# Kernel optimization log

Hardware: AMD Instinct MI355X
Metric: run time of the kernel (lower is better)

The kernel has to match this reference:

```python
import jax, jax.numpy as jnp
import numpy as np

EMBED_DIM = 1024
NUM_HEADS = 16
HEAD_DIM = EMBED_DIM // NUM_HEADS
B, S = 8, 1024


def setup_inputs() -> dict:
    key = jax.random.key(0)
    ks = jax.random.split(key, 8)
    scale = 1.0 / np.sqrt(EMBED_DIM)
    return {
        "q": jax.random.normal(ks[0], (B, S, EMBED_DIM), jnp.float32),
        "v": jax.random.normal(ks[1], (B, S, EMBED_DIM), jnp.float32),
        "Wq": jax.random.normal(ks[2], (EMBED_DIM, EMBED_DIM), jnp.float32) * scale,
        "bq": jnp.zeros((EMBED_DIM,), jnp.float32),
        "Wk": jax.random.normal(ks[3], (EMBED_DIM, EMBED_DIM), jnp.float32) * scale,
        "bk": jnp.zeros((EMBED_DIM,), jnp.float32),
        "Wv": jax.random.normal(ks[4], (EMBED_DIM, EMBED_DIM), jnp.float32) * scale,
        "bv": jnp.zeros((EMBED_DIM,), jnp.float32),
    }


def reference(q, v, Wq, bq, Wk, bk, Wv, bv):
    # call(q, v, k=None): k defaults to v, then compute_multihead_attention(q, v, k)
    # maps (q_arg=q, k_arg=v, v_arg=v) in self-attention.
    qp = q @ Wq + bq                     # [B, S, E]
    kp = v @ Wk + bk                     # [B, S, E]
    vp = v @ Wv + bv                     # [B, S, E]
    # split along feature dim into heads (same math as tf.split+concat on batch)
    qh = qp.reshape(B, S, NUM_HEADS, HEAD_DIM)
    kh = kp.reshape(B, S, NUM_HEADS, HEAD_DIM)
    vh = vp.reshape(B, S, NUM_HEADS, HEAD_DIM)
    # NOTE: original scales by 1/sqrt(embed_dim), not 1/sqrt(head_dim)
    scores = jnp.einsum("bqhd,bkhd->bhqk", qh, kh) / np.sqrt(EMBED_DIM)
    att = jax.nn.softmax(scores, axis=-1)
    out = jnp.einsum("bhqk,bkhd->bqhd", att, vh)  # [B, S, H, Dh]
    return out.reshape(B, S, EMBED_DIM)
```

## Files before the change

### kernel.cpp

```cpp
#include <hip/hip_runtime.h>
#include <cstdint>
#include <cstddef>

#define E 1024
#define S 1024
#define NB 8
#define NH 16
#define DH 64

typedef __bf16 bf16_t;
typedef __bf16 bf16x8 __attribute__((ext_vector_type(8)));
typedef __bf16 bf16x4 __attribute__((ext_vector_type(4)));
typedef __bf16 bf16x2 __attribute__((ext_vector_type(2)));
typedef short s16x4 __attribute__((ext_vector_type(4)));
typedef float f32x4 __attribute__((ext_vector_type(4)));

static __device__ __forceinline__ void gload_lds16(const void* g, void* l) {
  __builtin_amdgcn_global_load_lds((const __attribute__((address_space(1))) void*)g,
                                   (__attribute__((address_space(3))) void*)l, 16, 0, 0);
}

static __device__ __forceinline__ float fast_exp2(float x) {
#if __has_builtin(__builtin_amdgcn_exp2f)
  return __builtin_amdgcn_exp2f(x);
#else
  float r;
  asm("v_exp_f32 %0, %1" : "=v"(r) : "v"(x));
  return r;
#endif
}

__global__ __launch_bounds__(256) void convert_kernel(
    const float* __restrict__ q, const float* __restrict__ v,
    bf16_t* __restrict__ qb, bf16_t* __restrict__ vb) {
  const float* src = blockIdx.y ? v : q;
  bf16_t* dst = blockIdx.y ? vb : qb;
  const size_t i = ((size_t)blockIdx.x * 256 + threadIdx.x) * 8;
  float4 a = *(const float4*)(src + i);
  float4 b = *(const float4*)(src + i + 4);
  bf16x8 o = {(bf16_t)a.x, (bf16_t)a.y, (bf16_t)a.z, (bf16_t)a.w,
              (bf16_t)b.x, (bf16_t)b.y, (bf16_t)b.z, (bf16_t)b.w};
  *(bf16x8*)(dst + i) = o;
}

__global__ void wtrans_kernel(const float* __restrict__ Wq, const float* __restrict__ Wk,
                              const float* __restrict__ Wv, bf16_t* __restrict__ Wqt,
                              bf16_t* __restrict__ Wkt, bf16_t* __restrict__ Wvt) {
  const float* W = (blockIdx.z == 0) ? Wq : (blockIdx.z == 1) ? Wk : Wv;
  bf16_t* Wt = (blockIdx.z == 0) ? Wqt : (blockIdx.z == 1) ? Wkt : Wvt;
  __shared__ float tile[32][33];
  const int n0 = blockIdx.x * 32, k0 = blockIdx.y * 32;
  const int tx = threadIdx.x, ty = threadIdx.y;
#pragma unroll
  for (int i = ty; i < 32; i += 8)
    tile[i][tx] = W[(size_t)(k0 + i) * E + n0 + tx];
  __syncthreads();
#pragma unroll
  for (int i = ty; i < 32; i += 8)
    Wt[(size_t)(n0 + i) * E + k0 + tx] = (bf16_t)tile[tx][i];
}

__global__ __launch_bounds__(256, 2) void gemm3_kernel(
    const bf16_t* __restrict__ qbf, const bf16_t* __restrict__ vbf,
    const bf16_t* __restrict__ Wqt, const bf16_t* __restrict__ Wkt,
    const bf16_t* __restrict__ Wvt, const float* __restrict__ bq,
    const float* __restrict__ bk, const float* __restrict__ bv,
    bf16_t* __restrict__ qp, bf16_t* __restrict__ kp, bf16_t* __restrict__ vp,
    float qscale) {
  extern __shared__ __align__(16) char smem[];

  const int t = threadIdx.x;
  const int wv = t >> 6, l = t & 63;
  const int lc = l & 15, lg = l >> 4;
  const int wc = wv;

  const int nt = blockIdx.y;
  const int sel = nt >> 2;
  const bf16_t* A = sel ? vbf : qbf;
  const bf16_t* Bt = (sel == 0) ? Wqt : (sel == 1) ? Wkt : Wvt;
  const float* bias = (sel == 0) ? bq : (sel == 1) ? bk : bv;
  bf16_t* C = (sel == 0) ? qp : (sel == 1) ? kp : vp;
  const float scale = (sel == 0) ? qscale : 1.0f;

  const int m0 = blockIdx.x * 128;
  const int n0 = (nt & 3) * 256;

  const int rr = t >> 2;
  const int sgE = ((((t & 3) + ((t >> 3) & 3)) & 3)) << 3;
  const bf16_t* aS0 = A + (size_t)(m0 + rr) * E + sgE;
  const bf16_t* aS1 = A + (size_t)(m0 + 64 + rr) * E + sgE;
  const bf16_t* bS0 = Bt + (size_t)(n0 + rr) * E + sgE;
  const bf16_t* bS1 = Bt + (size_t)(n0 + 64 + rr) * E + sgE;
  const bf16_t* bS2 = Bt + (size_t)(n0 + 128 + rr) * E + sgE;
  const bf16_t* bS3 = Bt + (size_t)(n0 + 192 + rr) * E + sgE;

#define STAGE(tile, buf)                          \
  {                                               \
    const int k0_ = (tile) * 32;                  \
    char* d_ = smem + (buf) * 24576 + wv * 1024;  \
    gload_lds16(aS0 + k0_, d_);                   \
    gload_lds16(aS1 + k0_, d_ + 4096);            \
    gload_lds16(bS0 + k0_, d_ + 8192);            \
    gload_lds16(bS1 + k0_, d_ + 12288);           \
    gload_lds16(bS2 + k0_, d_ + 16384);           \
    gload_lds16(bS3 + k0_, d_ + 20480);           \
  }

  const int cRd = ((lg - (lc >> 1)) & 3) << 4;
  const int aRowB = lc * 64 + cRd;
  const int bRowB = 8192 + (wc * 64 + lc) * 64 + cRd;

  f32x4 acc[8][4] = {};

  STAGE(0, 0);
  STAGE(1, 1);
  asm volatile("s_waitcnt vmcnt(6)" ::: "memory");
  asm volatile("s_barrier" ::: "memory");

  int bufC = 0, bufS = 2;
  for (int tk = 0; tk < 32; ++tk) {
    const char* base = smem + bufC * 24576;
    if (tk + 2 < 32) STAGE(tk + 2, bufS);

    bf16x8 fa[8], fb[4];
#pragma unroll
    for (int ni = 0; ni < 4; ++ni)
      fb[ni] = *(const bf16x8*)(base + bRowB + ni * 1024);
#pragma unroll
    for (int mi = 0; mi < 8; ++mi)
      fa[mi] = *(const bf16x8*)(base + aRowB + mi * 1024);

    __builtin_amdgcn_s_setprio(1);
#pragma unroll
    for (int mi = 0; mi < 8; ++mi)
#pragma unroll
      for (int ni = 0; ni < 4; ++ni)
        acc[mi][ni] = __builtin_amdgcn_mfma_f32_16x16x32_bf16(fa[mi], fb[ni], acc[mi][ni], 0, 0, 0);
    __builtin_amdgcn_s_setprio(0);

    if (tk + 2 < 32) {
      asm volatile("s_waitcnt vmcnt(6)" ::: "memory");
    } else if (tk == 30) {
      asm volatile("s_waitcnt vmcnt(0)" ::: "memory");
    }
    if (tk < 31) asm volatile("s_barrier" ::: "memory");
    bufC = (bufC == 2) ? 0 : bufC + 1;
    bufS = (bufS == 2) ? 0 : bufS + 1;
  }
#undef STAGE

#pragma unroll
  for (int ni = 0; ni < 4; ++ni) {
    const int n = n0 + wc * 64 + ni * 16 + lc;
    const float bv_ = bias[n];
#pragma unroll
    for (int mi = 0; mi < 8; ++mi) {
#pragma unroll
      for (int r = 0; r < 4; ++r) {
        const int m = m0 + mi * 16 + lg * 4 + r;
        C[(size_t)m * E + n] = (bf16_t)((acc[mi][ni][r] + bv_) * scale);
      }
    }
  }
}

#if __has_builtin(__builtin_amdgcn_mfma_f32_16x16x16bf16_1k)
static __device__ __forceinline__ f32x4 mfma16(s16x4 a, s16x4 b, f32x4 c) {
  return __builtin_amdgcn_mfma_f32_16x16x16bf16_1k(a, b, c, 0, 0, 0);
}
#else
static __device__ __forceinline__ f32x4 mfma16(s16x4 a, s16x4 b, f32x4 c) {
  asm volatile("v_mfma_f32_16x16x16_bf16 %0, %1, %2, %0" : "+v"(c) : "v"(a), "v"(b));
  return c;
}
#endif

__global__ __launch_bounds__(256, 2) void attn_kernel(
    const bf16_t* __restrict__ qp, const bf16_t* __restrict__ kp,
    const bf16_t* __restrict__ vp, float* __restrict__ out) {
  __shared__ __align__(16) unsigned char KsB[2][64 * 128];
  __shared__ bf16_t Vs[2][64][72];
  const int t = threadIdx.x;
  const int w = t >> 6, l = t & 63;
  const int lc = l & 15, lg = l >> 4;

  const int swz = (blockIdx.x & 7) * 64 + (blockIdx.x >> 3);
  const int qblk = swz & 3, bh = swz >> 2;
  const int h = bh & 15, b = bh >> 4;
  const int qbase = qblk * 256 + w * 64;
  const size_t bh_off = (size_t)b * S * E + (size_t)h * DH;

  bf16x8 qf[4][2];
#pragma unroll
  for (int qi = 0; qi < 4; ++qi)
#pragma unroll
    for (int kc = 0; kc < 2; ++kc)
      qf[qi][kc] = *(const bf16x8*)(qp + bh_off + (size_t)(qbase + 16 * qi + lc) * E + kc * 32 + lg * 8);

  f32x4 po[4][4] = {};
  float l_[4] = {0.f, 0.f, 0.f, 0.f};

  const int krow = t >> 2, kc4 = t & 3;
  const int vkv2 = (t & 31) * 2, vd0 = (t >> 5) * 8;
  const bf16_t* kbase = kp + bh_off;
  const bf16_t* vbase = vp + bh_off;
  const int ksw = (krow & 7) << 4;

  bf16x8 ka0, ka1, va0, va1;
  {
    const bf16_t* ks = kbase + (size_t)krow * E + kc4 * 16;
    ka0 = *(const bf16x8*)ks;
    ka1 = *(const bf16x8*)(ks + 8);
    const bf16_t* vs = vbase + (size_t)vkv2 * E + vd0;
    va0 = *(const bf16x8*)vs;
    va1 = *(const bf16x8*)(vs + E);
    *(bf16x8*)&KsB[0][krow * 128 + ((kc4 * 32) ^ ksw)] = ka0;
    *(bf16x8*)&KsB[0][krow * 128 + ((kc4 * 32 + 16) ^ ksw)] = ka1;
#pragma unroll
    for (int j = 0; j < 8; ++j) {
      bf16x2 pr;
      pr[0] = va0[j];
      pr[1] = va1[j];
      *(bf16x2*)&Vs[0][vd0 + j][vkv2] = pr;
    }
  }
  int cur = 0;

  for (int kv0 = 0; kv0 < S; kv0 += 64) {
    __syncthreads();

    const bool more = (kv0 + 64 < S);
    if (more) {
      const bf16_t* ks = kbase + (size_t)(kv0 + 64 + krow) * E + kc4 * 16;
      ka0 = *(const bf16x8*)ks;
      ka1 = *(const bf16x8*)(ks + 8);
      const bf16_t* vs = vbase + (size_t)(kv0 + 64 + vkv2) * E + vd0;
      va0 = *(const bf16x8*)vs;
      va1 = *(const bf16x8*)(vs + E);
    }

    s16x4 pa[4][4];
    __builtin_amdgcn_s_setprio(1);
#pragma unroll
    for (int kvb = 0; kvb < 4; ++kvb) {
      const int row = kvb * 16 + lc;
      const int sw = (lc & 7) << 4;
      bf16x8 ak0 = *(const bf16x8*)&KsB[cur][row * 128 + ((lg * 16) ^ sw)];
      bf16x8 ak1 = *(const bf16x8*)&KsB[cur][row * 128 + ((64 + lg * 16) ^ sw)];
      f32x4 sc[4] = {};
#pragma unroll
      for (int qi = 0; qi < 4; ++qi) {
        sc[qi] = __builtin_amdgcn_mfma_f32_16x16x32_bf16(ak0, qf[qi][0], sc[qi], 0, 0, 0);
        sc[qi] = __builtin_amdgcn_mfma_f32_16x16x32_bf16(ak1, qf[qi][1], sc[qi], 0, 0, 0);
      }
#pragma unroll
      for (int qi = 0; qi < 4; ++qi) {
        const float e0 = fast_exp2(sc[qi][0]);
        const float e1 = fast_exp2(sc[qi][1]);
        const float e2 = fast_exp2(sc[qi][2]);
        const float e3 = fast_exp2(sc[qi][3]);
        l_[qi] += (e0 + e1) + (e2 + e3);
        bf16x4 pb = {(bf16_t)e0, (bf16_t)e1, (bf16_t)e2, (bf16_t)e3};
        pa[qi][kvb] = *(s16x4*)&pb;
      }
    }

#pragma unroll
    for (int ki = 0; ki < 4; ++ki) {
      s16x4 av[4];
#pragma unroll
      for (int ni = 0; ni < 4; ++ni)
        av[ni] = *(const s16x4*)&Vs[cur][16 * ni + lc][16 * ki + lg * 4];
#pragma unroll
      for (int qi = 0; qi < 4; ++qi)
#pragma unroll
        for (int ni = 0; ni < 4; ++ni)
          po[qi][ni] = mfma16(av[ni], pa[qi][ki], po[qi][ni]);
    }
    __builtin_amdgcn_s_setprio(0);

    if (more) {
      const int nb_ = cur ^ 1;
      *(bf16x8*)&KsB[nb_][krow * 128 + ((kc4 * 32) ^ ksw)] = ka0;
      *(bf16x8*)&KsB[nb_][krow * 128 + ((kc4 * 32 + 16) ^ ksw)] = ka1;
#pragma unroll
      for (int j = 0; j < 8; ++j) {
        bf16x2 pr;
        pr[0] = va0[j];
        pr[1] = va1[j];
        *(bf16x2*)&Vs[nb_][vd0 + j][vkv2] = pr;
      }
      cur = nb_;
    }
  }

#pragma unroll
  for (int qi = 0; qi < 4; ++qi) {
    float lt = l_[qi];
    lt += __shfl_xor(lt, 16, 64);
    lt += __shfl_xor(lt, 32, 64);
    const float inv = 1.0f / lt;
    const int qrow = qbase + 16 * qi + lc;
    float* op = out + (size_t)b * S * E + (size_t)qrow * E + h * DH;
#pragma unroll
    for (int ni = 0; ni < 4; ++ni) {
      f32x4 r = po[qi][ni] * inv;
      *(f32x4*)(op + 16 * ni + lg * 4) = r;
    }
  }
}

extern "C" void kernel_launch(void* const* d_in, const int* in_sizes, int n_in,
                              void* d_out, int out_size, void* d_ws, size_t ws_size,
                              hipStream_t stream) {
  const float* q  = (const float*)d_in[0];
  const float* v  = (const float*)d_in[1];
  const float* Wq = (const float*)d_in[2];
  const float* bq = (const float*)d_in[3];
  const float* Wk = (const float*)d_in[4];
  const float* bk = (const float*)d_in[5];
  const float* Wv = (const float*)d_in[6];
  const float* bv = (const float*)d_in[7];
  float* out = (float*)d_out;

  char* ws = (char*)d_ws;
  bf16_t* Wqt = (bf16_t*)(ws);
  bf16_t* Wkt = (bf16_t*)(ws + (size_t)2 * 1024 * 1024);
  bf16_t* Wvt = (bf16_t*)(ws + (size_t)4 * 1024 * 1024);
  bf16_t* qp  = (bf16_t*)(ws + (size_t)6 * 1024 * 1024);
  bf16_t* kp  = (bf16_t*)(ws + (size_t)22 * 1024 * 1024);
  bf16_t* vp  = (bf16_t*)(ws + (size_t)38 * 1024 * 1024);

  bf16_t* qbf = (bf16_t*)d_out;
  bf16_t* vbf = qbf + (size_t)NB * S * E;

  (void)hipFuncSetAttribute((const void*)gemm3_kernel,
                            hipFuncAttributeMaxDynamicSharedMemorySize, 73728);

  convert_kernel<<<dim3(4096, 2), 256, 0, stream>>>(q, v, qbf, vbf);
  wtrans_kernel<<<dim3(32, 32, 3), dim3(32, 8), 0, stream>>>(Wq, Wk, Wv, Wqt, Wkt, Wvt);

  const float qscale = 0.03125f * 1.44269504088896f;
  gemm3_kernel<<<dim3(64, 12), 256, 73728, stream>>>(qbf, vbf, Wqt, Wkt, Wvt,
                                                     bq, bk, bv, qp, kp, vp, qscale);
  attn_kernel<<<dim3(512), 256, 0, stream>>>(qp, kp, vp, out);
}
```

Measured before the change: 135.3 us.

## Fuse fp32-to-bf16 input conversion into projection GEMM and use 16x16x32 MFMA for PV

```diff
diff --git a/kernel.cpp b/kernel.cpp
--- a/kernel.cpp
+++ b/kernel.cpp
@@ -30,19 +30,6 @@
 #endif
 }
 
-__global__ __launch_bounds__(256) void convert_kernel(
-    const float* __restrict__ q, const float* __restrict__ v,
-    bf16_t* __restrict__ qb, bf16_t* __restrict__ vb) {
-  const float* src = blockIdx.y ? v : q;
-  bf16_t* dst = blockIdx.y ? vb : qb;
-  const size_t i = ((size_t)blockIdx.x * 256 + threadIdx.x) * 8;
-  float4 a = *(const float4*)(src + i);
-  float4 b = *(const float4*)(src + i + 4);
-  bf16x8 o = {(bf16_t)a.x, (bf16_t)a.y, (bf16_t)a.z, (bf16_t)a.w,
-              (bf16_t)b.x, (bf16_t)b.y, (bf16_t)b.z, (bf16_t)b.w};
-  *(bf16x8*)(dst + i) = o;
-}
-
 __global__ void wtrans_kernel(const float* __restrict__ Wq, const float* __restrict__ Wk,
                               const float* __restrict__ Wv, bf16_t* __restrict__ Wqt,
                               bf16_t* __restrict__ Wkt, bf16_t* __restrict__ Wvt) {
@@ -61,7 +48,7 @@
 }
 
 __global__ __launch_bounds__(256, 2) void gemm3_kernel(
-    const bf16_t* __restrict__ qbf, const bf16_t* __restrict__ vbf,
+    const float* __restrict__ qf32, const float* __restrict__ vf32,
     const bf16_t* __restrict__ Wqt, const bf16_t* __restrict__ Wkt,
     const bf16_t* __restrict__ Wvt, const float* __restrict__ bq,
     const float* __restrict__ bk, const float* __restrict__ bv,
@@ -76,7 +63,7 @@
 
   const int nt = blockIdx.y;
   const int sel = nt >> 2;
-  const bf16_t* A = sel ? vbf : qbf;
+  const float* A = sel ? vf32 : qf32;
   const bf16_t* Bt = (sel == 0) ? Wqt : (sel == 1) ? Wkt : Wvt;
   const float* bias = (sel == 0) ? bq : (sel == 1) ? bk : bv;
   bf16_t* C = (sel == 0) ? qp : (sel == 1) ? kp : vp;
@@ -86,24 +73,54 @@
   const int n0 = (nt & 3) * 256;
 
   const int rr = t >> 2;
-  const int sgE = ((((t & 3) + ((t >> 3) & 3)) & 3)) << 3;
-  const bf16_t* aS0 = A + (size_t)(m0 + rr) * E + sgE;
-  const bf16_t* aS1 = A + (size_t)(m0 + 64 + rr) * E + sgE;
-  const bf16_t* bS0 = Bt + (size_t)(n0 + rr) * E + sgE;
-  const bf16_t* bS1 = Bt + (size_t)(n0 + 64 + rr) * E + sgE;
-  const bf16_t* bS2 = Bt + (size_t)(n0 + 128 + rr) * E + sgE;
-  const bf16_t* bS3 = Bt + (size_t)(n0 + 192 + rr) * E + sgE;
-
-#define STAGE(tile, buf)                          \
+  const int sg = ((t & 3) + ((t >> 3) & 3)) & 3;
+  const float* aF0 = A + (size_t)(m0 + rr) * E + sg * 8;
+  const float* aF1 = A + (size_t)(m0 + 64 + rr) * E + sg * 8;
+  const bf16_t* bS0 = Bt + (size_t)(n0 + rr) * E + sg * 8;
+  const bf16_t* bS1 = Bt + (size_t)(n0 + 64 + rr) * E + sg * 8;
+  const bf16_t* bS2 = Bt + (size_t)(n0 + 128 + rr) * E + sg * 8;
+  const bf16_t* bS3 = Bt + (size_t)(n0 + 192 + rr) * E + sg * 8;
+  char* const aw0base = smem + t * 16;
+  char* const aw1base = smem + 4096 + t * 16;
+
+  f32x4 raE[4], raO[4];
+
+#define AISSUE(ra, tile)                          \
+  {                                               \
+    const float* f0_ = aF0 + (tile) * 32;         \
+    const float* f1_ = aF1 + (tile) * 32;         \
+    ra[0] = *(const f32x4*)f0_;                   \
+    ra[1] = *(const f32x4*)(f0_ + 4);             \
+    ra[2] = *(const f32x4*)f1_;                   \
+    ra[3] = *(const f32x4*)(f1_ + 4);             \
+  }
+
+#define AWRITE(ra, buf)                                                      \
+  {                                                                          \
+    bf16x8 w0_ = {(bf16_t)ra[0][0], (bf16_t)ra[0][1], (bf16_t)ra[0][2],      \
+                  (bf16_t)ra[0][3], (bf16_t)ra[1][0], (bf16_t)ra[1][1],      \
+                  (bf16_t)ra[1][2], (bf16_t)ra[1][3]};                       \
+    bf16x8 w1_ = {(bf16_t)ra[2][0], (bf16_t)ra[2][1], (bf16_t)ra[2][2],      \
+                  (bf16_t)ra[2][3], (bf16_t)ra[3][0], (bf16_t)ra[3][1],      \
+                  (bf16_t)ra[3][2], (bf16_t)ra[3][3]};                       \
+    *(bf16x8*)(aw0base + (buf) * 24576) = w0_;                               \
+    *(bf16x8*)(aw1base + (buf) * 24576) = w1_;                               \
+  }
+
+#define BSTAGE(tile, buf)                         \
   {                                               \
     const int k0_ = (tile) * 32;                  \
-    char* d_ = smem + (buf) * 24576 + wv * 1024;  \
-    gload_lds16(aS0 + k0_, d_);                   \
-    gload_lds16(aS1 + k0_, d_ + 4096);            \
-    gload_lds16(bS0 + k0_, d_ + 8192);            \
-    gload_lds16(bS1 + k0_, d_ + 12288);           \
-    gload_lds16(bS2 + k0_, d_ + 16384);           \
-    gload_lds16(bS3 + k0_, d_ + 20480);           \
+    char* d_ = smem + (buf) * 24576 + 8192 + wv * 1024; \
+    gload_lds16(bS0 + k0_, d_);                   \
+    gload_lds16(bS1 + k0_, d_ + 4096);            \
+    gload_lds16(bS2 + k0_, d_ + 8192);            \
+    gload_lds16(bS3 + k0_, d_ + 12288);           \
+  }
+
+#define BARW()                                              \
+  {                                                         \
+    asm volatile("s_waitcnt lgkmcnt(0)" ::: "memory");      \
+    __builtin_amdgcn_s_barrier();                           \
   }
 
   const int cRd = ((lg - (lc >> 1)) & 3) << 4;
@@ -112,42 +129,68 @@
 
   f32x4 acc[8][4] = {};
 
-  STAGE(0, 0);
-  STAGE(1, 1);
-  asm volatile("s_waitcnt vmcnt(6)" ::: "memory");
-  asm volatile("s_barrier" ::: "memory");
-
-  int bufC = 0, bufS = 2;
-  for (int tk = 0; tk < 32; ++tk) {
-    const char* base = smem + bufC * 24576;
-    if (tk + 2 < 32) STAGE(tk + 2, bufS);
-
-    bf16x8 fa[8], fb[4];
-#pragma unroll
-    for (int ni = 0; ni < 4; ++ni)
-      fb[ni] = *(const bf16x8*)(base + bRowB + ni * 1024);
-#pragma unroll
-    for (int mi = 0; mi < 8; ++mi)
-      fa[mi] = *(const bf16x8*)(base + aRowB + mi * 1024);
-
-    __builtin_amdgcn_s_setprio(1);
-#pragma unroll
-    for (int mi = 0; mi < 8; ++mi)
-#pragma unroll
-      for (int ni = 0; ni < 4; ++ni)
-        acc[mi][ni] = __builtin_amdgcn_mfma_f32_16x16x32_bf16(fa[mi], fb[ni], acc[mi][ni], 0, 0, 0);
-    __builtin_amdgcn_s_setprio(0);
-
+#define COMPUTE(base)                                                        \
+  {                                                                          \
+    bf16x8 fa[8], fb[4];                                                     \
+    _Pragma("unroll") for (int ni = 0; ni < 4; ++ni)                         \
+        fb[ni] = *(const bf16x8*)((base) + bRowB + ni * 1024);               \
+    _Pragma("unroll") for (int mi = 0; mi < 8; ++mi)                         \
+        fa[mi] = *(const bf16x8*)((base) + aRowB + mi * 1024);               \
+    __builtin_amdgcn_s_setprio(1);                                           \
+    _Pragma("unroll") for (int mi = 0; mi < 8; ++mi)                         \
+        _Pragma("unroll") for (int ni = 0; ni < 4; ++ni)                     \
+            acc[mi][ni] = __builtin_amdgcn_mfma_f32_16x16x32_bf16(           \
+                fa[mi], fb[ni], acc[mi][ni], 0, 0, 0);                       \
+    __builtin_amdgcn_s_setprio(0);                                           \
+  }
+
+  AISSUE(raE, 0);
+  BSTAGE(0, 0);
+  AISSUE(raO, 1);
+  BSTAGE(1, 1);
+  asm volatile("s_waitcnt vmcnt(12)" ::: "memory");
+  AWRITE(raE, 0);
+  asm volatile("s_waitcnt vmcnt(8)" ::: "memory");
+  BARW();
+
+  int bc = 0;
+  for (int tk = 0; tk < 32; tk += 2) {
+    const int b1 = (bc + 1 == 3) ? 0 : bc + 1;
+    const int b2 = (b1 + 1 == 3) ? 0 : b1 + 1;
     if (tk + 2 < 32) {
-      asm volatile("s_waitcnt vmcnt(6)" ::: "memory");
-    } else if (tk == 30) {
+      AISSUE(raE, tk + 2);
+      BSTAGE(tk + 2, b2);
+    }
+    COMPUTE(smem + bc * 24576);
+    if (tk + 2 < 32) {
+      asm volatile("s_waitcnt vmcnt(12)" ::: "memory");
+      AWRITE(raO, b1);
+      asm volatile("s_waitcnt vmcnt(8)" ::: "memory");
+      BARW();
+    } else {
+      asm volatile("s_waitcnt vmcnt(4)" ::: "memory");
+      AWRITE(raO, b1);
       asm volatile("s_waitcnt vmcnt(0)" ::: "memory");
-    }
-    if (tk < 31) asm volatile("s_barrier" ::: "memory");
-    bufC = (bufC == 2) ? 0 : bufC + 1;
-    bufS = (bufS == 2) ? 0 : bufS + 1;
-  }
-#undef STAGE
+      BARW();
+    }
+    if (tk + 3 < 32) {
+      AISSUE(raO, tk + 3);
+      BSTAGE(tk + 3, bc);
+    }
+    COMPUTE(smem + b1 * 24576);
+    if (tk + 3 < 32) {
+      asm volatile("s_waitcnt vmcnt(12)" ::: "memory");
+      AWRITE(raE, b2);
+      asm volatile("s_waitcnt vmcnt(8)" ::: "memory");
+      BARW();
+    }
+    bc = b2;
+  }
+#undef COMPUTE
+#undef BARW
+#undef BSTAGE
+#undef AWRITE
+#undef AISSUE
 
 #pragma unroll
   for (int ni = 0; ni < 4; ++ni) {
@@ -163,17 +206,6 @@
     }
   }
 }
-
-#if __has_builtin(__builtin_amdgcn_mfma_f32_16x16x16bf16_1k)
-static __device__ __forceinline__ f32x4 mfma16(s16x4 a, s16x4 b, f32x4 c) {
-  return __builtin_amdgcn_mfma_f32_16x16x16bf16_1k(a, b, c, 0, 0, 0);
-}
-#else
-static __device__ __forceinline__ f32x4 mfma16(s16x4 a, s16x4 b, f32x4 c) {
-  asm volatile("v_mfma_f32_16x16x16_bf16 %0, %1, %2, %0" : "+v"(c) : "v"(a), "v"(b));
-  return c;
-}
-#endif
 
 __global__ __launch_bounds__(256, 2) void attn_kernel(
     const bf16_t* __restrict__ qp, const bf16_t* __restrict__ kp,
@@ -239,7 +271,7 @@
       va1 = *(const bf16x8*)(vs + E);
     }
 
-    s16x4 pa[4][4];
+    bf16x8 pa2[4][2];
     __builtin_amdgcn_s_setprio(1);
 #pragma unroll
     for (int kvb = 0; kvb < 4; ++kvb) {
@@ -260,22 +292,28 @@
         const float e2 = fast_exp2(sc[qi][2]);
         const float e3 = fast_exp2(sc[qi][3]);
         l_[qi] += (e0 + e1) + (e2 + e3);
-        bf16x4 pb = {(bf16_t)e0, (bf16_t)e1, (bf16_t)e2, (bf16_t)e3};
-        pa[qi][kvb] = *(s16x4*)&pb;
-      }
-    }
-
-#pragma unroll
-    for (int ki = 0; ki < 4; ++ki) {
-      s16x4 av[4];
-#pragma unroll
-      for (int ni = 0; ni < 4; ++ni)
-        av[ni] = *(const s16x4*)&Vs[cur][16 * ni + lc][16 * ki + lg * 4];
+        const int hi = (kvb & 1) * 4;
+        pa2[qi][kvb >> 1][hi + 0] = (bf16_t)e0;
+        pa2[qi][kvb >> 1][hi + 1] = (bf16_t)e1;
+        pa2[qi][kvb >> 1][hi + 2] = (bf16_t)e2;
+        pa2[qi][kvb >> 1][hi + 3] = (bf16_t)e3;
+      }
+    }
+
+#pragma unroll
+    for (int ki = 0; ki < 2; ++ki) {
+      bf16x8 av[4];
+#pragma unroll
+      for (int ni = 0; ni < 4; ++ni) {
+        const bf16x4 vlo = *(const bf16x4*)&Vs[cur][16 * ni + lc][32 * ki + 4 * lg];
+        const bf16x4 vhi = *(const bf16x4*)&Vs[cur][16 * ni + lc][32 * ki + 16 + 4 * lg];
+        av[ni] = __builtin_shufflevector(vlo, vhi, 0, 1, 2, 3, 4, 5, 6, 7);
+      }
 #pragma unroll
       for (int qi = 0; qi < 4; ++qi)
 #pragma unroll
         for (int ni = 0; ni < 4; ++ni)
-          po[qi][ni] = mfma16(av[ni], pa[qi][ki], po[qi][ni]);
+          po[qi][ni] = __builtin_amdgcn_mfma_f32_16x16x32_bf16(av[ni], pa2[qi][ki], po[qi][ni], 0, 0, 0);
     }
     __builtin_amdgcn_s_setprio(0);
 
@@ -331,17 +369,13 @@
   bf16_t* kp  = (bf16_t*)(ws + (size_t)22 * 1024 * 1024);
   bf16_t* vp  = (bf16_t*)(ws + (size_t)38 * 1024 * 1024);
 
-  bf16_t* qbf = (bf16_t*)d_out;
-  bf16_t* vbf = qbf + (size_t)NB * S * E;
-
   (void)hipFuncSetAttribute((const void*)gemm3_kernel,
                             hipFuncAttributeMaxDynamicSharedMemorySize, 73728);
 
-  convert_kernel<<<dim3(4096, 2), 256, 0, stream>>>(q, v, qbf, vbf);
   wtrans_kernel<<<dim3(32, 32, 3), dim3(32, 8), 0, stream>>>(Wq, Wk, Wv, Wqt, Wkt, Wvt);
 
   const float qscale = 0.03125f * 1.44269504088896f;
-  gemm3_kernel<<<dim3(64, 12), 256, 73728, stream>>>(qbf, vbf, Wqt, Wkt, Wvt,
+  gemm3_kernel<<<dim3(64, 12), 256, 73728, stream>>>(q, v, Wqt, Wkt, Wvt,
                                                      bq, bk, bv, qp, kp, vp, qscale);
   attn_kernel<<<dim3(512), 256, 0, stream>>>(qp, kp, vp, out);
 }
```

Measured after the change: 118.7 us. 12.3% less time.

## Merge prep kernels and use 16x16x32 MFMA for PV product

Applied to the files above, without the earlier changes.

```diff
diff --git a/kernel.cpp b/kernel.cpp
--- a/kernel.cpp
+++ b/kernel.cpp
@@ -30,27 +30,31 @@
 #endif
 }
 
-__global__ __launch_bounds__(256) void convert_kernel(
+__global__ __launch_bounds__(256) void prep_kernel(
     const float* __restrict__ q, const float* __restrict__ v,
-    bf16_t* __restrict__ qb, bf16_t* __restrict__ vb) {
-  const float* src = blockIdx.y ? v : q;
-  bf16_t* dst = blockIdx.y ? vb : qb;
-  const size_t i = ((size_t)blockIdx.x * 256 + threadIdx.x) * 8;
-  float4 a = *(const float4*)(src + i);
-  float4 b = *(const float4*)(src + i + 4);
-  bf16x8 o = {(bf16_t)a.x, (bf16_t)a.y, (bf16_t)a.z, (bf16_t)a.w,
-              (bf16_t)b.x, (bf16_t)b.y, (bf16_t)b.z, (bf16_t)b.w};
-  *(bf16x8*)(dst + i) = o;
-}
-
-__global__ void wtrans_kernel(const float* __restrict__ Wq, const float* __restrict__ Wk,
-                              const float* __restrict__ Wv, bf16_t* __restrict__ Wqt,
-                              bf16_t* __restrict__ Wkt, bf16_t* __restrict__ Wvt) {
-  const float* W = (blockIdx.z == 0) ? Wq : (blockIdx.z == 1) ? Wk : Wv;
-  bf16_t* Wt = (blockIdx.z == 0) ? Wqt : (blockIdx.z == 1) ? Wkt : Wvt;
+    const float* __restrict__ Wq, const float* __restrict__ Wk,
+    const float* __restrict__ Wv, bf16_t* __restrict__ qb, bf16_t* __restrict__ vb,
+    bf16_t* __restrict__ Wqt, bf16_t* __restrict__ Wkt, bf16_t* __restrict__ Wvt) {
+  const int t = threadIdx.x;
+  if (blockIdx.y < 2) {
+    const float* src = blockIdx.y ? v : q;
+    bf16_t* dst = blockIdx.y ? vb : qb;
+    const size_t i = ((size_t)blockIdx.x * 256 + t) * 8;
+    float4 a = *(const float4*)(src + i);
+    float4 b = *(const float4*)(src + i + 4);
+    bf16x8 o = {(bf16_t)a.x, (bf16_t)a.y, (bf16_t)a.z, (bf16_t)a.w,
+                (bf16_t)b.x, (bf16_t)b.y, (bf16_t)b.z, (bf16_t)b.w};
+    *(bf16x8*)(dst + i) = o;
+    return;
+  }
+  const int x = blockIdx.x;
+  if (x >= 3072) return;
+  const int z = x >> 10, rem = x & 1023;
+  const float* W = (z == 0) ? Wq : (z == 1) ? Wk : Wv;
+  bf16_t* Wt = (z == 0) ? Wqt : (z == 1) ? Wkt : Wvt;
   __shared__ float tile[32][33];
-  const int n0 = blockIdx.x * 32, k0 = blockIdx.y * 32;
-  const int tx = threadIdx.x, ty = threadIdx.y;
+  const int n0 = (rem >> 5) * 32, k0 = (rem & 31) * 32;
+  const int tx = t & 31, ty = t >> 5;
 #pragma unroll
   for (int i = ty; i < 32; i += 8)
     tile[i][tx] = W[(size_t)(k0 + i) * E + n0 + tx];
@@ -164,17 +168,6 @@
   }
 }
 
-#if __has_builtin(__builtin_amdgcn_mfma_f32_16x16x16bf16_1k)
-static __device__ __forceinline__ f32x4 mfma16(s16x4 a, s16x4 b, f32x4 c) {
-  return __builtin_amdgcn_mfma_f32_16x16x16bf16_1k(a, b, c, 0, 0, 0);
-}
-#else
-static __device__ __forceinline__ f32x4 mfma16(s16x4 a, s16x4 b, f32x4 c) {
-  asm volatile("v_mfma_f32_16x16x16_bf16 %0, %1, %2, %0" : "+v"(c) : "v"(a), "v"(b));
-  return c;
-}
-#endif
-
 __global__ __launch_bounds__(256, 2) void attn_kernel(
     const bf16_t* __restrict__ qp, const bf16_t* __restrict__ kp,
     const bf16_t* __restrict__ vp, float* __restrict__ out) {
@@ -239,7 +232,7 @@
       va1 = *(const bf16x8*)(vs + E);
     }
 
-    s16x4 pa[4][4];
+    bf16x8 pa2[4][2];
     __builtin_amdgcn_s_setprio(1);
 #pragma unroll
     for (int kvb = 0; kvb < 4; ++kvb) {
@@ -260,22 +253,28 @@
         const float e2 = fast_exp2(sc[qi][2]);
         const float e3 = fast_exp2(sc[qi][3]);
         l_[qi] += (e0 + e1) + (e2 + e3);
-        bf16x4 pb = {(bf16_t)e0, (bf16_t)e1, (bf16_t)e2, (bf16_t)e3};
-        pa[qi][kvb] = *(s16x4*)&pb;
-      }
-    }
-
-#pragma unroll
-    for (int ki = 0; ki < 4; ++ki) {
-      s16x4 av[4];
-#pragma unroll
-      for (int ni = 0; ni < 4; ++ni)
-        av[ni] = *(const s16x4*)&Vs[cur][16 * ni + lc][16 * ki + lg * 4];
+        const int hi = (kvb & 1) * 4;
+        pa2[qi][kvb >> 1][hi + 0] = (bf16_t)e0;
+        pa2[qi][kvb >> 1][hi + 1] = (bf16_t)e1;
+        pa2[qi][kvb >> 1][hi + 2] = (bf16_t)e2;
+        pa2[qi][kvb >> 1][hi + 3] = (bf16_t)e3;
+      }
+    }
+
+#pragma unroll
+    for (int ki = 0; ki < 2; ++ki) {
+      bf16x8 av[4];
+#pragma unroll
+      for (int ni = 0; ni < 4; ++ni) {
+        const bf16x4 vlo = *(const bf16x4*)&Vs[cur][16 * ni + lc][32 * ki + 4 * lg];
+        const bf16x4 vhi = *(const bf16x4*)&Vs[cur][16 * ni + lc][32 * ki + 16 + 4 * lg];
+        av[ni] = __builtin_shufflevector(vlo, vhi, 0, 1, 2, 3, 4, 5, 6, 7);
+      }
 #pragma unroll
       for (int qi = 0; qi < 4; ++qi)
 #pragma unroll
         for (int ni = 0; ni < 4; ++ni)
-          po[qi][ni] = mfma16(av[ni], pa[qi][ki], po[qi][ni]);
+          po[qi][ni] = __builtin_amdgcn_mfma_f32_16x16x32_bf16(av[ni], pa2[qi][ki], po[qi][ni], 0, 0, 0);
     }
     __builtin_amdgcn_s_setprio(0);
 
@@ -337,8 +336,8 @@
   (void)hipFuncSetAttribute((const void*)gemm3_kernel,
                             hipFuncAttributeMaxDynamicSharedMemorySize, 73728);
 
-  convert_kernel<<<dim3(4096, 2), 256, 0, stream>>>(q, v, qbf, vbf);
-  wtrans_kernel<<<dim3(32, 32, 3), dim3(32, 8), 0, stream>>>(Wq, Wk, Wv, Wqt, Wkt, Wvt);
+  prep_kernel<<<dim3(4096, 3), 256, 0, stream>>>(q, v, Wq, Wk, Wv,
+                                                 qbf, vbf, Wqt, Wkt, Wvt);
 
   const float qscale = 0.03125f * 1.44269504088896f;
   gemm3_kernel<<<dim3(64, 12), 256, 73728, stream>>>(qbf, vbf, Wqt, Wkt, Wvt,
```

Measured after the change: 121.5 us. -10.2%, faster.
